# Kernel optimization log

Hardware: AMD Instinct MI355X
Metric: run time of the kernel (lower is better)

Reference implementation:

```python
import jax, jax.numpy as jnp
import numpy as np

NUM_CLASSES = 21
EPS = 1e-6
MOMENTUM = 0.99
K_WEAK = 16
K_STRONG = 256
PROB_THRESH = 0.95
IGNORE = 255
NEG = -1e30


def _normalize(x, axis=-1):
    # matches F.normalize(p=2) / CosineSimilarity with eps=1e-6
    n = jnp.linalg.norm(x, axis=axis, keepdims=True)
    return x / jnp.maximum(n, EPS)


def setup_inputs() -> dict:
    key = jax.random.key(0)
    k0, k1, k2, k3, k4, k5 = jax.random.split(key, 6)
    B, C, H, W = 8, 256, 128, 128
    feature_weak = jax.random.normal(k0, (B, C, H, W), jnp.float32)
    feature_strong = jax.random.normal(k1, (B, C, H, W), jnp.float32)
    probablity_weak = jax.random.uniform(k2, (B, H, W), jnp.float32)
    memory_bank = jax.random.normal(k3, (NUM_CLASSES, 1, C), jnp.float32)
    pred_weak = jax.random.randint(k4, (B, H, W), 0, NUM_CLASSES)
    ignore_mask = jax.random.randint(k5, (B, H, W), 0, 256)
    return {
        'feature_weak': feature_weak,
        'feature_strong': feature_strong,
        'probablity_weak': probablity_weak,
        'memory_bank': memory_bank,
        'pred_weak': pred_weak,
        'ignore_mask': ignore_mask,
    }


def reference(feature_weak, feature_strong, probablity_weak, memory_bank, pred_weak, ignore_mask):
    B, C, H, W = feature_weak.shape
    N = B * H * W
    fw = feature_weak.transpose(0, 2, 3, 1).reshape(N, C)   # weak pixel feats
    fs = feature_strong.transpose(0, 2, 3, 1).reshape(N, C) # strong pixel feats
    seg = pred_weak.reshape(N)
    ign = ignore_mask.reshape(N)  # same-size bilinear resize (align_corners) is identity
    prob = probablity_weak.reshape(N)

    valid = ign != IGNORE
    conf = valid & (prob > PROB_THRESH)

    cls = jnp.arange(NUM_CLASSES)
    is_cls = seg[None, :] == cls[:, None]        # [K, N]
    m_weak = is_cls & conf[None, :]              # per-class high-confidence mask
    m_strong = is_cls & valid[None, :]
    n_weak = m_weak.sum(axis=1)                  # [K]
    n_strong = m_strong.sum(axis=1)

    protos = memory_bank[:, 0, :]                # [K, C]
    pn = _normalize(protos)
    sim_w = _normalize(fw) @ pn.T                # [N, K] cos(pixel_weak, proto)
    sim_s = _normalize(fs) @ pn.T                # [N, K] cos(pixel_strong, proto)

    sw = jnp.where(m_weak, sim_w.T, NEG)         # [K, N]
    ss = jnp.where(m_strong, -sim_s.T, NEG)      # negate -> bottom-k via top_k
    _, idx_w = jax.lax.top_k(sw, K_WEAK)         # [K, 16] most-similar weak pixels
    _, idx_s = jax.lax.top_k(ss, K_STRONG)       # [K, 256] least-similar strong pixels

    # select_feature duplicates the top element: slots are ranks [0,0,1,...,14]
    ranks = jnp.maximum(jnp.arange(K_WEAK) - 1, 0)
    sel_w = fw[idx_w[:, ranks]]                  # [K, 16, C]
    sel_s = fs[idx_s]                            # [K, 256, C]

    kw = jnp.minimum(K_WEAK, n_weak)
    ks = jnp.minimum(K_STRONG, n_strong)
    valid_w = jnp.arange(K_WEAK)[None, :] < kw[:, None]     # [K, 16]
    valid_s = jnp.arange(K_STRONG)[None, :] < ks[:, None]   # [K, 256]

    # calculate_loss: weak side detached, max over strong dim, sum / strong count
    wn = _normalize(jax.lax.stop_gradient(sel_w))
    sn = _normalize(sel_s)
    cosm = jnp.einsum('kwc,ksc->kws', wn, sn)    # [K, 16, 256]
    cosm = jnp.where(valid_s[:, None, :], cosm, NEG)
    max_sim = jnp.where(valid_w, cosm.max(axis=2), 0.0)     # [K, 16]
    class_ok = (n_weak > 0) & (n_strong > 0)
    sim_sum = jnp.where(class_ok, max_sim.sum(axis=1), 0.0).sum()
    count = jnp.where(class_ok, ks, 0).sum()
    loss = jnp.where(count > 0, 1.0 - sim_sum / count, 0.0)

    # update_memory: per-class mean of high-confidence weak feats, EMA scatter
    fw_ng = jax.lax.stop_gradient(fw)            # .data copy -> no grad
    wsum = m_weak.astype(fw.dtype) @ fw_ng       # [K, C] segmented sum
    mean = wsum / jnp.maximum(n_weak, 1).astype(fw.dtype)[:, None]
    new_protos = jnp.where((n_weak > 0)[:, None],
                           MOMENTUM * protos + (1.0 - MOMENTUM) * mean,
                           protos)
    new_memory_bank = new_protos[:, None, :]     # [K, 1, C]
    return loss, new_memory_bank
```

## Files before the change

### kernel.cpp

```cpp
#include <hip/hip_runtime.h>
#include <stdint.h>

#define NCLS  21
#define CDIM  256
#define HWSZ  16384
#define NPIX  131072
#define EPSV  1e-6f
#define NEGV  -1e30f
#define CAP_W 4096
#define CAP_S 16384
#define KSEL  256
#define NCC   8
#define CCH   (CDIM/NCC)
#define NPART 8
#define NBLK2 (NPIX/512)
#define P2    2048
#define NPG   (NPIX/P2)

__device__ __forceinline__ uint64_t pack_key(float v, unsigned idx) {
  unsigned u = __float_as_uint(v);
  u = (u & 0x80000000u) ? ~u : (u | 0x80000000u);
  return ((uint64_t)(~u) << 32) | (uint64_t)idx;
}

__global__ void k0_init(const float* __restrict__ mb, float* pn, float* wsum) {
  int k = blockIdx.x, t = threadIdx.x;
  float v = mb[k * CDIM + t];
  float s = v * v;
  for (int o = 32; o > 0; o >>= 1) s += __shfl_down(s, o, 64);
  __shared__ float wsh[4];
  int wid = t >> 6, lane = t & 63;
  if (lane == 0) wsh[wid] = s;
  __syncthreads();
  float tot = wsh[0] + wsh[1] + wsh[2] + wsh[3];
  float inv = 1.0f / fmaxf(sqrtf(tot), EPSV);
  pn[k * CDIM + t] = v * inv;
  wsum[k * CDIM + t] = 0.0f;
}

__global__ __launch_bounds__(256, 2)
void k1a_stream(const float* __restrict__ fw, const float* __restrict__ fs,
                const float* __restrict__ prob, const int* __restrict__ seg,
                const int* __restrict__ ign, const float* __restrict__ pn,
                float* part, float* wsum) {
  __shared__ float pnT[CCH * NCLS];
  __shared__ float wloc[NCLS * (CCH + 1)];
  int t = threadIdx.x;
  int pg = blockIdx.x;
  int cc = blockIdx.y;
  int c0 = cc * CCH;
  for (int i = t; i < CCH * NCLS; i += 256) {
    int c = i / NCLS, k = i % NCLS;
    pnT[i] = pn[k * CDIM + c0 + c];
  }
  for (int i = t; i < NCLS * (CCH + 1); i += 256) wloc[i] = 0.0f;
  __syncthreads();

  int base = pg * P2;
  int b = base >> 14;
  int hwb = (base & (HWSZ - 1)) + t;

  int sgv[8]; bool cf[8];
  float dw[8], nw[8], dsv[8], nsv[8];
#pragma unroll
  for (int i = 0; i < 8; ++i) {
    int px = base + i * 256 + t;
    sgv[i] = seg[px];
    int igv = ign[px];
    float prv = prob[px];
    cf[i] = (igv != 255) && (prv > 0.95f);
    dw[i] = nw[i] = dsv[i] = nsv[i] = 0.0f;
  }

  const float* fwp = fw + ((size_t)b * CDIM + c0) * HWSZ + hwb;
  const float* fsp = fs + ((size_t)b * CDIM + c0) * HWSZ + hwb;

#pragma unroll 4
  for (int c = 0; c < CCH; ++c) {
    size_t co = (size_t)c * HWSZ;
    float a[8], s8[8];
#pragma unroll
    for (int i = 0; i < 8; ++i) a[i] = fwp[co + i * 256];
#pragma unroll
    for (int i = 0; i < 8; ++i) s8[i] = fsp[co + i * 256];
#pragma unroll
    for (int i = 0; i < 8; ++i) {
      float p = pnT[c * NCLS + sgv[i]];
      dw[i]  = fmaf(a[i],  p,     dw[i]);
      nw[i]  = fmaf(a[i],  a[i],  nw[i]);
      dsv[i] = fmaf(s8[i], p,     dsv[i]);
      nsv[i] = fmaf(s8[i], s8[i], nsv[i]);
      if (cf[i]) atomicAdd(&wloc[sgv[i] * (CCH + 1) + c], a[i]);
    }
  }

  float4* pp = (float4*)part + (size_t)cc * NPIX + base + t;
#pragma unroll
  for (int i = 0; i < 8; ++i)
    pp[i * 256] = make_float4(dw[i], nw[i], dsv[i], nsv[i]);

  __syncthreads();
  for (int i = t; i < NCLS * CCH; i += 256) {
    int k = i / CCH, cl = i % CCH;
    float v = wloc[k * (CCH + 1) + cl];
    if (v != 0.0f) atomicAdd(&wsum[k * CDIM + c0 + cl], v);
  }
}

__global__ void k1c_count(const float* __restrict__ prob, const int* __restrict__ seg,
                          const int* __restrict__ ign, int* cnts) {
  __shared__ int hs[NCLS], hw2[NCLS];
  int t = threadIdx.x, pg = blockIdx.x;
  for (int i = t; i < NCLS; i += 256) { hs[i] = 0; hw2[i] = 0; }
  __syncthreads();
  int n0 = pg * 512 + t * 2;
  int2   sg = *(const int2*)(seg + n0);
  int2   ig = *(const int2*)(ign + n0);
  float2 pr = *(const float2*)(prob + n0);
  bool v0 = (ig.x != 255), v1 = (ig.y != 255);
  if (v0) atomicAdd(&hs[sg.x], 1);
  if (v1) atomicAdd(&hs[sg.y], 1);
  if (v0 && pr.x > 0.95f) atomicAdd(&hw2[sg.x], 1);
  if (v1 && pr.y > 0.95f) atomicAdd(&hw2[sg.y], 1);
  __syncthreads();
  for (int i = t; i < NCLS; i += 256) {
    cnts[pg * NCLS + i] = hs[i];
    cnts[NBLK2 * NCLS + pg * NCLS + i] = hw2[i];
  }
}

__global__ void ks_scan(const int* __restrict__ cnts, int* offs, int* scnt, int* wcnt) {
  __shared__ int L[2 * NBLK2 * NCLS];
  int t = threadIdx.x;
  for (int i = t; i < 2 * NBLK2 * NCLS; i += 256) L[i] = cnts[i];
  __syncthreads();
  if (t < 2 * NCLS) {
    int q = t % NCLS;
    int typ = t / NCLS;
    int base = typ * NBLK2 * NCLS;
    int run = 0;
    for (int b2 = 0; b2 < NBLK2; ++b2) {
      int v = L[base + b2 * NCLS + q];
      L[base + b2 * NCLS + q] = run;
      run += v;
    }
    if (typ == 0) scnt[q] = run; else wcnt[q] = run;
  }
  __syncthreads();
  for (int i = t; i < 2 * NBLK2 * NCLS; i += 256) offs[i] = L[i];
}

__global__ void k1b_write(const float* __restrict__ part, const float* __restrict__ prob,
                          const int* __restrict__ seg, const int* __restrict__ ign,
                          const int* __restrict__ offs, uint64_t* wkeys, uint64_t* skeys) {
  __shared__ int ls[NCLS], lw[NCLS];
  int t = threadIdx.x, pg = blockIdx.x;
  if (t < NCLS) {
    ls[t] = offs[pg * NCLS + t];
    lw[t] = offs[NBLK2 * NCLS + pg * NCLS + t];
  }
  __syncthreads();
  int n0 = pg * 512 + t * 2;
  int2   sg = *(const int2*)(seg + n0);
  int2   ig = *(const int2*)(ign + n0);
  float2 pr = *(const float2*)(prob + n0);
  float dw[2] = {0,0}, nw[2] = {0,0}, ds[2] = {0,0}, ns[2] = {0,0};
#pragma unroll
  for (int cc = 0; cc < NCC; ++cc) {
    const float4* pp = (const float4*)part + ((size_t)cc * NPIX + n0);
#pragma unroll
    for (int i = 0; i < 2; ++i) {
      float4 v = pp[i];
      dw[i] += v.x; nw[i] += v.y; ds[i] += v.z; ns[i] += v.w;
    }
  }
  int   sga[2] = {sg.x, sg.y};
  int   iga[2] = {ig.x, ig.y};
  float pra[2] = {pr.x, pr.y};
#pragma unroll
  for (int i = 0; i < 2; ++i) {
    if (iga[i] != 255) {
      int q = sga[i];
      float sim_s = ds[i] / fmaxf(sqrtf(ns[i]), EPSV);
      int pos = atomicAdd(&ls[q], 1);
      if (pos < CAP_S) skeys[(size_t)q * CAP_S + pos] = pack_key(-sim_s, (unsigned)(n0 + i));
      if (pra[i] > 0.95f) {
        float sim_w = dw[i] / fmaxf(sqrtf(nw[i]), EPSV);
        int pw = atomicAdd(&lw[q], 1);
        if (pw < CAP_W) wkeys[(size_t)q * CAP_W + pw] = pack_key(sim_w, (unsigned)(n0 + i));
      }
    }
  }
}

__device__ void select_topk(const uint64_t* __restrict__ list, int cnt,
                            uint64_t* T, uint64_t* P, int* pcnt, int* woff) {
  int t = threadIdx.x;
  T[t] = ~0ull;
  if (t == 0) *pcnt = 0;
  __syncthreads();
  for (int base = 0; base < cnt; base += 256) {
    uint64_t key = (base + t < cnt) ? list[base + t] : ~0ull;
    uint64_t cutoff = T[KSEL - 1];
    bool pred = key < cutoff;
    unsigned long long mask = __ballot(pred);
    int wid = t >> 6, lane = t & 63;
    if (lane == 0) woff[wid] = __popcll(mask);
    int prefix = __popcll(mask & ((1ull << lane) - 1ull));
    __syncthreads();
    int off = 0;
    for (int w2 = 0; w2 < wid; ++w2) off += woff[w2];
    int total = woff[0] + woff[1] + woff[2] + woff[3];
    int old = *pcnt;
    if (pred) P[old + off + prefix] = key;
    int newc = old + total;
    __syncthreads();
    if (t == 0) *pcnt = newc;
    bool last = (base + 256 >= cnt);
    if (newc >= KSEL || (last && newc > 0)) {
      for (int i2 = t; i2 < 2 * KSEL; i2 += 256)
        if (i2 >= newc) P[i2] = ~0ull;
      for (unsigned size = 2; size <= 2 * KSEL; size <<= 1) {
        for (unsigned stride = size >> 1; stride > 0; stride >>= 1) {
          __syncthreads();
          unsigned lo = stride - 1;
          unsigned i = (((unsigned)t & ~lo) << 1) | ((unsigned)t & lo);
          unsigned j = i | stride;
          uint64_t a = P[i], b = P[j];
          bool up = ((i & size) == 0);
          if ((a > b) == up) { P[i] = b; P[j] = a; }
        }
      }
      __syncthreads();
      uint64_t a = T[t], b = P[KSEL - 1 - t];
      T[t] = a < b ? a : b;
      for (unsigned stride = KSEL / 2; stride > 0; stride >>= 1) {
        __syncthreads();
        if (((unsigned)t & stride) == 0) {
          uint64_t x = T[t], y = T[t + stride];
          if (x > y) { T[t] = y; T[t + stride] = x; }
        }
      }
      __syncthreads();
      if (t == 0) *pcnt = 0;
      __syncthreads();
    } else {
      __syncthreads();
    }
  }
}

__global__ void k2_topk(const uint64_t* __restrict__ wkeys, const uint64_t* __restrict__ skeys,
                        const int* wcnt, const int* scnt,
                        uint64_t* psel, int* idxw, int* kwv, int* nwv) {
  __shared__ uint64_t T[KSEL];
  __shared__ uint64_t P[2 * KSEL];
  __shared__ int pcnt;
  __shared__ int woff[4];
  int bid = blockIdx.x, t = threadIdx.x;
  if (bid < NCLS * NPART) {
    int k = bid / NPART, p = bid % NPART;
    int cnt = min(scnt[k], CAP_S);
    int chunk = (cnt + NPART - 1) / NPART;
    int lo = p * chunk;
    int hi = min(lo + chunk, cnt);
    int c = hi > lo ? hi - lo : 0;
    select_topk(skeys + (size_t)k * CAP_S + lo, c, T, P, &pcnt, woff);
    psel[((size_t)k * NPART + p) * KSEL + t] = T[t];
  } else {
    int k = bid - NCLS * NPART;
    int cnt_total = wcnt[k];
    int cnt = min(cnt_total, CAP_W);
    select_topk(wkeys + (size_t)k * CAP_W, cnt, T, P, &pcnt, woff);
    if (t < 16) idxw[k * 16 + t] = (int)(unsigned)(T[t] & 0xFFFFFFFFull);
    if (t == 0) { nwv[k] = cnt_total; kwv[k] = min(cnt_total, 16); }
  }
}

__global__ void k2m_merge(const uint64_t* __restrict__ psel, const int* scnt,
                          int* idxs, int* ksv, int* nsv) {
  int k = blockIdx.x, t = threadIdx.x;
  __shared__ uint64_t M[NPART * KSEL];
  __shared__ uint64_t M2[4 * KSEL];
  for (int i = t; i < NPART * KSEL; i += 256) M[i] = psel[(size_t)k * NPART * KSEL + i];
  __syncthreads();
#pragma unroll
  for (int p = 0; p < 4; ++p) {
    uint64_t a = M[p * 512 + t], b = M[p * 512 + 511 - t];
    M2[p * 256 + t] = a < b ? a : b;
  }
  for (int str = 128; str > 0; str >>= 1) {
    __syncthreads();
    for (int q = t; q < 4 * 128; q += 256) {
      int list = q >> 7, r = q & 127;
      int i = ((r & ~(str - 1)) << 1) | (r & (str - 1));
      int ai = list * 256 + i, bi = ai + str;
      uint64_t x = M2[ai], y = M2[bi];
      if (x > y) { M2[ai] = y; M2[bi] = x; }
    }
  }
  __syncthreads();
#pragma unroll
  for (int p = 0; p < 2; ++p) {
    uint64_t a = M2[p * 512 + t], b = M2[p * 512 + 511 - t];
    M[p * 256 + t] = a < b ? a : b;
  }
  for (int str = 128; str > 0; str >>= 1) {
    __syncthreads();
    {
      int q = t;
      int list = q >> 7, r = q & 127;
      int i = ((r & ~(str - 1)) << 1) | (r & (str - 1));
      int ai = list * 256 + i, bi = ai + str;
      uint64_t x = M[ai], y = M[bi];
      if (x > y) { M[ai] = y; M[bi] = x; }
    }
  }
  __syncthreads();
  {
    uint64_t a = M[t], b = M[511 - t];
    M2[t] = a < b ? a : b;
  }
  for (int str = 128; str > 0; str >>= 1) {
    __syncthreads();
    if (t < 128) {
      int r = t;
      int i = ((r & ~(str - 1)) << 1) | (r & (str - 1));
      uint64_t x = M2[i], y = M2[i + str];
      if (x > y) { M2[i] = y; M2[i + str] = x; }
    }
  }
  __syncthreads();
  idxs[k * KSEL + t] = (int)(unsigned)(M2[t] & 0xFFFFFFFFull);
  if (t == 0) { int c = scnt[k]; nsv[k] = c; ksv[k] = c < KSEL ? c : KSEL; }
}

__global__ void k3a_gather(const float* __restrict__ fw, const float* __restrict__ fs,
                           const int* __restrict__ idxw, const int* __restrict__ idxs,
                           const int* __restrict__ kwv, const int* __restrict__ ksv,
                           float* dw_dense, float* ds_dense) {
  int k = blockIdx.y;
  int s0 = blockIdx.x * 4;
  int t = threadIdx.x;
  int wid = t >> 6, lane = t & 63;
  float v[4];
  bool strong[4];
  int slot_[4];
#pragma unroll
  for (int j = 0; j < 4; ++j) {
    int slot = s0 + j;
    slot_[j] = slot;
    strong[j] = slot < KSEL;
    bool ok;
    int n = 0;
    if (strong[j]) {
      ok = slot < ksv[k];
      if (ok) n = idxs[k * KSEL + slot];
    } else {
      int i = slot - KSEL;
      ok = i < kwv[k];
      int rank = i > 0 ? i - 1 : 0;
      if (ok) n = idxw[k * 16 + rank];
    }
    v[j] = 0.0f;
    if (ok) {
      int b = n >> 14, hw = n & (HWSZ - 1);
      const float* f = strong[j] ? fs : fw;
      v[j] = f[(size_t)(b * CDIM + t) * HWSZ + hw];
    }
  }
  __shared__ float wsh[4][4];
  float s[4];
#pragma unroll
  for (int j = 0; j < 4; ++j) {
    s[j] = v[j] * v[j];
    for (int o = 32; o > 0; o >>= 1) s[j] += __shfl_down(s[j], o, 64);
  }
  if (lane == 0) {
#pragma unroll
    for (int j = 0; j < 4; ++j) wsh[wid][j] = s[j];
  }
  __syncthreads();
#pragma unroll
  for (int j = 0; j < 4; ++j) {
    float tot = wsh[0][j] + wsh[1][j] + wsh[2][j] + wsh[3][j];
    float inv = 1.0f / fmaxf(sqrtf(tot), EPSV);
    float out = v[j] * inv;
    if (strong[j]) ds_dense[((size_t)k * KSEL + slot_[j]) * CDIM + t] = out;
    else           dw_dense[((size_t)k * 16 + (slot_[j] - KSEL)) * CDIM + t] = out;
  }
}

__global__ void k3b_loss(const float* __restrict__ dw_dense, const float* __restrict__ ds_dense,
                         const int* kwv, const int* ksv, const int* nwv, const int* nsv,
                         float* simsum, int* countk) {
  int k = blockIdx.x, t = threadIdx.x;
  int wid = t >> 6, lane = t & 63;
  __shared__ float wn[16 * CDIM];
  __shared__ float wred[4][16];
  for (int i = t; i < 16 * CDIM; i += 256) wn[i] = dw_dense[(size_t)k * 16 * CDIM + i];
  __syncthreads();
  int ks_ = ksv[k], kw_ = kwv[k];
  bool ok = (nwv[k] > 0) && (nsv[k] > 0);
  float dots[16];
#pragma unroll
  for (int i = 0; i < 16; ++i) dots[i] = 0.0f;
  bool jv = ok && (t < ks_);
  if (jv) {
    const float4* sp = (const float4*)(ds_dense + ((size_t)k * KSEL + t) * CDIM);
    for (int c4 = 0; c4 < CDIM / 4; ++c4) {
      float4 v = sp[c4];
#pragma unroll
      for (int i = 0; i < 16; ++i) {
        float4 w = ((const float4*)(wn + i * CDIM))[c4];
        dots[i] = fmaf(v.x, w.x, dots[i]);
        dots[i] = fmaf(v.y, w.y, dots[i]);
        dots[i] = fmaf(v.z, w.z, dots[i]);
        dots[i] = fmaf(v.w, w.w, dots[i]);
      }
    }
  }
#pragma unroll
  for (int i = 0; i < 16; ++i) {
    float v = jv ? dots[i] : NEGV;
    for (int o = 32; o > 0; o >>= 1) v = fmaxf(v, __shfl_down(v, o, 64));
    if (lane == 0) wred[wid][i] = v;
  }
  __syncthreads();
  if (t == 0) {
    float csum = 0.0f;
    for (int i = 0; i < kw_; ++i) {
      float m = fmaxf(fmaxf(wred[0][i], wred[1][i]), fmaxf(wred[2][i], wred[3][i]));
      csum += m;
    }
    simsum[k] = ok ? csum : 0.0f;
    countk[k] = ok ? ks_ : 0;
  }
}

__global__ void k4_final(const float* __restrict__ mb, const float* __restrict__ wsum,
                         const int* __restrict__ nwv, const float* __restrict__ simsum,
                         const int* __restrict__ countk, float* out) {
  int k = blockIdx.x, t = threadIdx.x;
  float p = mb[k * CDIM + t];
  float o = p;
  int nw = nwv[k];
  if (nw > 0) {
    float mean = wsum[k * CDIM + t] / (float)nw;
    o = 0.99f * p + 0.01f * mean;
  }
  out[1 + k * CDIM + t] = o;
  if (k == 0 && t == 0) {
    float ss = 0.0f;
    int cc = 0;
    for (int q = 0; q < NCLS; ++q) { ss += simsum[q]; cc += countk[q]; }
    out[0] = (cc > 0) ? (1.0f - ss / (float)cc) : 0.0f;
  }
}

extern "C" void kernel_launch(void* const* d_in, const int* in_sizes, int n_in,
                              void* d_out, int out_size, void* d_ws, size_t ws_size,
                              hipStream_t stream) {
  const float* fw   = (const float*)d_in[0];
  const float* fs   = (const float*)d_in[1];
  const float* prob = (const float*)d_in[2];
  const float* mb   = (const float*)d_in[3];
  const int*   seg  = (const int*)d_in[4];
  const int*   ign  = (const int*)d_in[5];
  float* out = (float*)d_out;

  char* ws = (char*)d_ws;
  size_t off = 0;
  auto alloc = [&](size_t bytes) -> char* {
    char* p = ws + off;
    off = (off + bytes + 255) & ~(size_t)255;
    return p;
  };
  float*    pn       = (float*)alloc(NCLS * CDIM * 4);
  float*    wsum     = (float*)alloc(NCLS * CDIM * 4);
  int*      wcnt     = (int*)alloc(NCLS * 4);
  int*      scnt     = (int*)alloc(NCLS * 4);
  int*      idxw     = (int*)alloc(NCLS * 16 * 4);
  int*      idxs     = (int*)alloc(NCLS * KSEL * 4);
  int*      kwv      = (int*)alloc(NCLS * 4);
  int*      ksv      = (int*)alloc(NCLS * 4);
  int*      nwv      = (int*)alloc(NCLS * 4);
  int*      nsv      = (int*)alloc(NCLS * 4);
  float*    simsum   = (float*)alloc(NCLS * 4);
  int*      countk   = (int*)alloc(NCLS * 4);
  int*      cnts     = (int*)alloc(2 * NBLK2 * NCLS * 4);
  int*      offs     = (int*)alloc(2 * NBLK2 * NCLS * 4);
  uint64_t* wkeys    = (uint64_t*)alloc((size_t)NCLS * CAP_W * 8);
  uint64_t* skeys    = (uint64_t*)alloc((size_t)NCLS * CAP_S * 8);
  uint64_t* psel     = (uint64_t*)alloc((size_t)NCLS * NPART * KSEL * 8);
  float*    dw_dense = (float*)alloc((size_t)NCLS * 16 * CDIM * 4);
  float*    ds_dense = (float*)alloc((size_t)NCLS * KSEL * CDIM * 4);
  float*    part     = (float*)alloc((size_t)NCC * NPIX * 4 * 4);
  (void)in_sizes; (void)n_in; (void)out_size; (void)ws_size;

  k0_init<<<NCLS, 256, 0, stream>>>(mb, pn, wsum);
  k1a_stream<<<dim3(NPG, NCC), 256, 0, stream>>>(fw, fs, prob, seg, ign, pn,
                                                 part, wsum);
  k1c_count<<<NBLK2, 256, 0, stream>>>(prob, seg, ign, cnts);
  ks_scan<<<1, 256, 0, stream>>>(cnts, offs, scnt, wcnt);
  k1b_write<<<NBLK2, 256, 0, stream>>>(part, prob, seg, ign, offs, wkeys, skeys);
  k2_topk<<<NCLS * NPART + NCLS, 256, 0, stream>>>(wkeys, skeys, wcnt, scnt,
                                                   psel, idxw, kwv, nwv);
  k2m_merge<<<NCLS, 256, 0, stream>>>(psel, scnt, idxs, ksv, nsv);
  k3a_gather<<<dim3((KSEL + 16) / 4, NCLS), 256, 0, stream>>>(fw, fs, idxw, idxs, kwv, ksv,
                                                              dw_dense, ds_dense);
  k3b_loss<<<NCLS, 256, 0, stream>>>(dw_dense, ds_dense, kwv, ksv, nwv, nsv,
                                     simsum, countk);
  k4_final<<<NCLS, 256, 0, stream>>>(mb, wsum, nwv, simsum, countk, out);
}
```

Measured before the change: 403.1 us.

## Fuse streaming, counting, scan and key-write into one kernel with atomic offsets

The channel-chunked streaming kernel, the per-block histogram, the single-block scan and the key-writing pass are merged into one kernel. Each block now processes 512 pixels across all 256 channels and claims per-class output slots through global atomics instead of a precomputed prefix scan. This removes the partial-dot-product buffer round trip and several launches. The loss step is also split across 4 smaller blocks per class, with the final reduction moved into the last kernel. In exchange the grid shrinks to 256 blocks with a long serial channel loop and roughly 43KB of shared memory per block, which may limit occupancy and memory-latency hiding. Key order within each class list becomes nondeterministic, though top-k ties break on pixel index.

```diff
diff --git a/kernel.cpp b/kernel.cpp
--- a/kernel.cpp
+++ b/kernel.cpp
@@ -10,12 +10,10 @@
 #define CAP_W 4096
 #define CAP_S 16384
 #define KSEL  256
-#define NCC   8
-#define CCH   (CDIM/NCC)
 #define NPART 8
-#define NBLK2 (NPIX/512)
-#define P2    2048
-#define NPG   (NPIX/P2)
+#define P2M   512
+#define NBLKM (NPIX/P2M)
+#define CPAD  (CDIM+1)
 
 __device__ __forceinline__ uint64_t pack_key(float v, unsigned idx) {
   unsigned u = __float_as_uint(v);
@@ -23,7 +21,8 @@
   return ((uint64_t)(~u) << 32) | (uint64_t)idx;
 }
 
-__global__ void k0_init(const float* __restrict__ mb, float* pn, float* wsum) {
+__global__ void k0_init(const float* __restrict__ mb, float* pn, float* wsum,
+                        int* wcnt, int* scnt) {
   int k = blockIdx.x, t = threadIdx.x;
   float v = mb[k * CDIM + t];
   float s = v * v;
@@ -36,160 +35,96 @@
   float inv = 1.0f / fmaxf(sqrtf(tot), EPSV);
   pn[k * CDIM + t] = v * inv;
   wsum[k * CDIM + t] = 0.0f;
-}
-
-__global__ __launch_bounds__(256, 2)
-void k1a_stream(const float* __restrict__ fw, const float* __restrict__ fs,
-                const float* __restrict__ prob, const int* __restrict__ seg,
-                const int* __restrict__ ign, const float* __restrict__ pn,
-                float* part, float* wsum) {
-  __shared__ float pnT[CCH * NCLS];
-  __shared__ float wloc[NCLS * (CCH + 1)];
-  int t = threadIdx.x;
-  int pg = blockIdx.x;
-  int cc = blockIdx.y;
-  int c0 = cc * CCH;
-  for (int i = t; i < CCH * NCLS; i += 256) {
+  if (k == 0 && t < 2 * NCLS) {
+    if (t < NCLS) wcnt[t] = 0; else scnt[t - NCLS] = 0;
+  }
+}
+
+__global__ __launch_bounds__(256)
+void k1a_mega(const float* __restrict__ fw, const float* __restrict__ fs,
+              const float* __restrict__ prob, const int* __restrict__ seg,
+              const int* __restrict__ ign, const float* __restrict__ pn,
+              float* wsum, int* wcnt, int* scnt,
+              uint64_t* wkeys, uint64_t* skeys) {
+  __shared__ float pnT[CDIM * NCLS];
+  __shared__ float wloc[NCLS * CPAD];
+  __shared__ int cw[NCLS], cs[NCLS], bw[NCLS], bs[NCLS];
+  int t = threadIdx.x, pg = blockIdx.x;
+  for (int i = t; i < CDIM * NCLS; i += 256) {
     int c = i / NCLS, k = i % NCLS;
-    pnT[i] = pn[k * CDIM + c0 + c];
-  }
-  for (int i = t; i < NCLS * (CCH + 1); i += 256) wloc[i] = 0.0f;
-  __syncthreads();
-
-  int base = pg * P2;
+    pnT[i] = pn[k * CDIM + c];
+  }
+  for (int i = t; i < NCLS * CPAD; i += 256) wloc[i] = 0.0f;
+  if (t < NCLS) { cw[t] = 0; cs[t] = 0; }
+  __syncthreads();
+
+  int base = pg * P2M;
   int b = base >> 14;
-  int hwb = (base & (HWSZ - 1)) + t;
-
-  int sgv[8]; bool cf[8];
-  float dw[8], nw[8], dsv[8], nsv[8];
-#pragma unroll
-  for (int i = 0; i < 8; ++i) {
-    int px = base + i * 256 + t;
-    sgv[i] = seg[px];
-    int igv = ign[px];
-    float prv = prob[px];
-    cf[i] = (igv != 255) && (prv > 0.95f);
-    dw[i] = nw[i] = dsv[i] = nsv[i] = 0.0f;
-  }
-
-  const float* fwp = fw + ((size_t)b * CDIM + c0) * HWSZ + hwb;
-  const float* fsp = fs + ((size_t)b * CDIM + c0) * HWSZ + hwb;
-
-#pragma unroll 4
-  for (int c = 0; c < CCH; ++c) {
-    size_t co = (size_t)c * HWSZ;
-    float a[8], s8[8];
-#pragma unroll
-    for (int i = 0; i < 8; ++i) a[i] = fwp[co + i * 256];
-#pragma unroll
-    for (int i = 0; i < 8; ++i) s8[i] = fsp[co + i * 256];
-#pragma unroll
-    for (int i = 0; i < 8; ++i) {
-      float p = pnT[c * NCLS + sgv[i]];
-      dw[i]  = fmaf(a[i],  p,     dw[i]);
-      nw[i]  = fmaf(a[i],  a[i],  nw[i]);
-      dsv[i] = fmaf(s8[i], p,     dsv[i]);
-      nsv[i] = fmaf(s8[i], s8[i], nsv[i]);
-      if (cf[i]) atomicAdd(&wloc[sgv[i] * (CCH + 1) + c], a[i]);
-    }
-  }
-
-  float4* pp = (float4*)part + (size_t)cc * NPIX + base + t;
-#pragma unroll
-  for (int i = 0; i < 8; ++i)
-    pp[i * 256] = make_float4(dw[i], nw[i], dsv[i], nsv[i]);
-
-  __syncthreads();
-  for (int i = t; i < NCLS * CCH; i += 256) {
-    int k = i / CCH, cl = i % CCH;
-    float v = wloc[k * (CCH + 1) + cl];
-    if (v != 0.0f) atomicAdd(&wsum[k * CDIM + c0 + cl], v);
-  }
-}
-
-__global__ void k1c_count(const float* __restrict__ prob, const int* __restrict__ seg,
-                          const int* __restrict__ ign, int* cnts) {
-  __shared__ int hs[NCLS], hw2[NCLS];
-  int t = threadIdx.x, pg = blockIdx.x;
-  for (int i = t; i < NCLS; i += 256) { hs[i] = 0; hw2[i] = 0; }
-  __syncthreads();
-  int n0 = pg * 512 + t * 2;
-  int2   sg = *(const int2*)(seg + n0);
-  int2   ig = *(const int2*)(ign + n0);
-  float2 pr = *(const float2*)(prob + n0);
-  bool v0 = (ig.x != 255), v1 = (ig.y != 255);
-  if (v0) atomicAdd(&hs[sg.x], 1);
-  if (v1) atomicAdd(&hs[sg.y], 1);
-  if (v0 && pr.x > 0.95f) atomicAdd(&hw2[sg.x], 1);
-  if (v1 && pr.y > 0.95f) atomicAdd(&hw2[sg.y], 1);
-  __syncthreads();
-  for (int i = t; i < NCLS; i += 256) {
-    cnts[pg * NCLS + i] = hs[i];
-    cnts[NBLK2 * NCLS + pg * NCLS + i] = hw2[i];
-  }
-}
-
-__global__ void ks_scan(const int* __restrict__ cnts, int* offs, int* scnt, int* wcnt) {
-  __shared__ int L[2 * NBLK2 * NCLS];
-  int t = threadIdx.x;
-  for (int i = t; i < 2 * NBLK2 * NCLS; i += 256) L[i] = cnts[i];
-  __syncthreads();
-  if (t < 2 * NCLS) {
-    int q = t % NCLS;
-    int typ = t / NCLS;
-    int base = typ * NBLK2 * NCLS;
-    int run = 0;
-    for (int b2 = 0; b2 < NBLK2; ++b2) {
-      int v = L[base + b2 * NCLS + q];
-      L[base + b2 * NCLS + q] = run;
-      run += v;
-    }
-    if (typ == 0) scnt[q] = run; else wcnt[q] = run;
-  }
-  __syncthreads();
-  for (int i = t; i < 2 * NBLK2 * NCLS; i += 256) offs[i] = L[i];
-}
-
-__global__ void k1b_write(const float* __restrict__ part, const float* __restrict__ prob,
-                          const int* __restrict__ seg, const int* __restrict__ ign,
-                          const int* __restrict__ offs, uint64_t* wkeys, uint64_t* skeys) {
-  __shared__ int ls[NCLS], lw[NCLS];
-  int t = threadIdx.x, pg = blockIdx.x;
+  int hw0 = (base & (HWSZ - 1)) + t;
+  int n0 = base + t, n1 = base + 256 + t;
+  int sg0 = seg[n0], sg1 = seg[n1];
+  int ig0 = ign[n0], ig1 = ign[n1];
+  float pr0 = prob[n0], pr1 = prob[n1];
+  bool va0 = (ig0 != 255), va1 = (ig1 != 255);
+  bool cf0 = va0 && (pr0 > 0.95f), cf1 = va1 && (pr1 > 0.95f);
+
+  const float* fwp = fw + (size_t)b * CDIM * HWSZ + hw0;
+  const float* fsp = fs + (size_t)b * CDIM * HWSZ + hw0;
+
+  float dw0 = 0, nw0 = 0, ds0 = 0, ns0 = 0;
+  float dw1 = 0, nw1 = 0, ds1 = 0, ns1 = 0;
+#pragma unroll 8
+  for (int c = 0; c < CDIM; ++c) {
+    size_t o = (size_t)c * HWSZ;
+    float a0 = __builtin_nontemporal_load(fwp + o);
+    float a1 = __builtin_nontemporal_load(fwp + o + 256);
+    float s0 = __builtin_nontemporal_load(fsp + o);
+    float s1 = __builtin_nontemporal_load(fsp + o + 256);
+    float p0 = pnT[c * NCLS + sg0];
+    float p1 = pnT[c * NCLS + sg1];
+    dw0 = fmaf(a0, p0, dw0); nw0 = fmaf(a0, a0, nw0);
+    ds0 = fmaf(s0, p0, ds0); ns0 = fmaf(s0, s0, ns0);
+    dw1 = fmaf(a1, p1, dw1); nw1 = fmaf(a1, a1, nw1);
+    ds1 = fmaf(s1, p1, ds1); ns1 = fmaf(s1, s1, ns1);
+    if (cf0) atomicAdd(&wloc[sg0 * CPAD + c], a0);
+    if (cf1) atomicAdd(&wloc[sg1 * CPAD + c], a1);
+  }
+
+  int ls0 = 0, lw0 = 0, ls1 = 0, lw1 = 0;
+  if (va0) ls0 = atomicAdd(&cs[sg0], 1);
+  if (va1) ls1 = atomicAdd(&cs[sg1], 1);
+  if (cf0) lw0 = atomicAdd(&cw[sg0], 1);
+  if (cf1) lw1 = atomicAdd(&cw[sg1], 1);
+  __syncthreads();
   if (t < NCLS) {
-    ls[t] = offs[pg * NCLS + t];
-    lw[t] = offs[NBLK2 * NCLS + pg * NCLS + t];
-  }
-  __syncthreads();
-  int n0 = pg * 512 + t * 2;
-  int2   sg = *(const int2*)(seg + n0);
-  int2   ig = *(const int2*)(ign + n0);
-  float2 pr = *(const float2*)(prob + n0);
-  float dw[2] = {0,0}, nw[2] = {0,0}, ds[2] = {0,0}, ns[2] = {0,0};
-#pragma unroll
-  for (int cc = 0; cc < NCC; ++cc) {
-    const float4* pp = (const float4*)part + ((size_t)cc * NPIX + n0);
-#pragma unroll
-    for (int i = 0; i < 2; ++i) {
-      float4 v = pp[i];
-      dw[i] += v.x; nw[i] += v.y; ds[i] += v.z; ns[i] += v.w;
-    }
-  }
-  int   sga[2] = {sg.x, sg.y};
-  int   iga[2] = {ig.x, ig.y};
-  float pra[2] = {pr.x, pr.y};
-#pragma unroll
-  for (int i = 0; i < 2; ++i) {
-    if (iga[i] != 255) {
-      int q = sga[i];
-      float sim_s = ds[i] / fmaxf(sqrtf(ns[i]), EPSV);
-      int pos = atomicAdd(&ls[q], 1);
-      if (pos < CAP_S) skeys[(size_t)q * CAP_S + pos] = pack_key(-sim_s, (unsigned)(n0 + i));
-      if (pra[i] > 0.95f) {
-        float sim_w = dw[i] / fmaxf(sqrtf(nw[i]), EPSV);
-        int pw = atomicAdd(&lw[q], 1);
-        if (pw < CAP_W) wkeys[(size_t)q * CAP_W + pw] = pack_key(sim_w, (unsigned)(n0 + i));
-      }
-    }
+    bs[t] = atomicAdd(&scnt[t], cs[t]);
+    bw[t] = atomicAdd(&wcnt[t], cw[t]);
+  }
+  __syncthreads();
+  if (va0) {
+    float sim_s = ds0 / fmaxf(sqrtf(ns0), EPSV);
+    int pos = bs[sg0] + ls0;
+    if (pos < CAP_S) skeys[(size_t)sg0 * CAP_S + pos] = pack_key(-sim_s, (unsigned)n0);
+    if (cf0) {
+      float sim_w = dw0 / fmaxf(sqrtf(nw0), EPSV);
+      int pw = bw[sg0] + lw0;
+      if (pw < CAP_W) wkeys[(size_t)sg0 * CAP_W + pw] = pack_key(sim_w, (unsigned)n0);
+    }
+  }
+  if (va1) {
+    float sim_s = ds1 / fmaxf(sqrtf(ns1), EPSV);
+    int pos = bs[sg1] + ls1;
+    if (pos < CAP_S) skeys[(size_t)sg1 * CAP_S + pos] = pack_key(-sim_s, (unsigned)n1);
+    if (cf1) {
+      float sim_w = dw1 / fmaxf(sqrtf(nw1), EPSV);
+      int pw = bw[sg1] + lw1;
+      if (pw < CAP_W) wkeys[(size_t)sg1 * CAP_W + pw] = pack_key(sim_w, (unsigned)n1);
+    }
+  }
+  for (int i = t; i < NCLS * CDIM; i += 256) {
+    int k = i >> 8, c = i & 255;
+    float v = wloc[k * CPAD + c];
+    if (v != 0.0f) atomicAdd(&wsum[k * CDIM + c], v);
   }
 }
 
@@ -252,7 +187,7 @@
 
 __global__ void k2_topk(const uint64_t* __restrict__ wkeys, const uint64_t* __restrict__ skeys,
                         const int* wcnt, const int* scnt,
-                        uint64_t* psel, int* idxw, int* kwv, int* nwv) {
+                        uint64_t* psel, int* idxw) {
   __shared__ uint64_t T[KSEL];
   __shared__ uint64_t P[2 * KSEL];
   __shared__ int pcnt;
@@ -269,16 +204,13 @@
     psel[((size_t)k * NPART + p) * KSEL + t] = T[t];
   } else {
     int k = bid - NCLS * NPART;
-    int cnt_total = wcnt[k];
-    int cnt = min(cnt_total, CAP_W);
+    int cnt = min(wcnt[k], CAP_W);
     select_topk(wkeys + (size_t)k * CAP_W, cnt, T, P, &pcnt, woff);
     if (t < 16) idxw[k * 16 + t] = (int)(unsigned)(T[t] & 0xFFFFFFFFull);
-    if (t == 0) { nwv[k] = cnt_total; kwv[k] = min(cnt_total, 16); }
-  }
-}
-
-__global__ void k2m_merge(const uint64_t* __restrict__ psel, const int* scnt,
-                          int* idxs, int* ksv, int* nsv) {
+  }
+}
+
+__global__ void k2m_merge(const uint64_t* __restrict__ psel, int* idxs) {
   int k = blockIdx.x, t = threadIdx.x;
   __shared__ uint64_t M[NPART * KSEL];
   __shared__ uint64_t M2[4 * KSEL];
@@ -332,17 +264,18 @@
   }
   __syncthreads();
   idxs[k * KSEL + t] = (int)(unsigned)(M2[t] & 0xFFFFFFFFull);
-  if (t == 0) { int c = scnt[k]; nsv[k] = c; ksv[k] = c < KSEL ? c : KSEL; }
 }
 
 __global__ void k3a_gather(const float* __restrict__ fw, const float* __restrict__ fs,
                            const int* __restrict__ idxw, const int* __restrict__ idxs,
-                           const int* __restrict__ kwv, const int* __restrict__ ksv,
+                           const int* __restrict__ wcnt, const int* __restrict__ scnt,
                            float* dw_dense, float* ds_dense) {
   int k = blockIdx.y;
   int s0 = blockIdx.x * 4;
   int t = threadIdx.x;
   int wid = t >> 6, lane = t & 63;
+  int kw_ = min(wcnt[k], 16);
+  int ks_ = min(scnt[k], KSEL);
   float v[4];
   bool strong[4];
   int slot_[4];
@@ -354,11 +287,11 @@
     bool ok;
     int n = 0;
     if (strong[j]) {
-      ok = slot < ksv[k];
+      ok = slot < ks_;
       if (ok) n = idxs[k * KSEL + slot];
     } else {
       int i = slot - KSEL;
-      ok = i < kwv[k];
+      ok = i < kw_;
       int rank = i > 0 ? i - 1 : 0;
       if (ok) n = idxw[k * 16 + rank];
     }
@@ -392,22 +325,19 @@
 }
 
 __global__ void k3b_loss(const float* __restrict__ dw_dense, const float* __restrict__ ds_dense,
-                         const int* kwv, const int* ksv, const int* nwv, const int* nsv,
-                         float* simsum, int* countk) {
-  int k = blockIdx.x, t = threadIdx.x;
-  int wid = t >> 6, lane = t & 63;
+                         const int* __restrict__ scnt, float* pmax) {
+  int p = blockIdx.x, k = blockIdx.y, t = threadIdx.x;
   __shared__ float wn[16 * CDIM];
-  __shared__ float wred[4][16];
-  for (int i = t; i < 16 * CDIM; i += 256) wn[i] = dw_dense[(size_t)k * 16 * CDIM + i];
-  __syncthreads();
-  int ks_ = ksv[k], kw_ = kwv[k];
-  bool ok = (nwv[k] > 0) && (nsv[k] > 0);
+  for (int i = t; i < 16 * CDIM; i += 64) wn[i] = dw_dense[(size_t)k * 16 * CDIM + i];
+  __syncthreads();
+  int ks_ = min(scnt[k], KSEL);
+  int slot = p * 64 + t;
+  bool jv = slot < ks_;
   float dots[16];
 #pragma unroll
   for (int i = 0; i < 16; ++i) dots[i] = 0.0f;
-  bool jv = ok && (t < ks_);
   if (jv) {
-    const float4* sp = (const float4*)(ds_dense + ((size_t)k * KSEL + t) * CDIM);
+    const float4* sp = (const float4*)(ds_dense + ((size_t)k * KSEL + slot) * CDIM);
     for (int c4 = 0; c4 < CDIM / 4; ++c4) {
       float4 v = sp[c4];
 #pragma unroll
@@ -424,37 +354,50 @@
   for (int i = 0; i < 16; ++i) {
     float v = jv ? dots[i] : NEGV;
     for (int o = 32; o > 0; o >>= 1) v = fmaxf(v, __shfl_down(v, o, 64));
-    if (lane == 0) wred[wid][i] = v;
-  }
-  __syncthreads();
-  if (t == 0) {
-    float csum = 0.0f;
-    for (int i = 0; i < kw_; ++i) {
-      float m = fmaxf(fmaxf(wred[0][i], wred[1][i]), fmaxf(wred[2][i], wred[3][i]));
-      csum += m;
-    }
-    simsum[k] = ok ? csum : 0.0f;
-    countk[k] = ok ? ks_ : 0;
+    if (t == 0) pmax[((size_t)k * 4 + p) * 16 + i] = v;
   }
 }
 
 __global__ void k4_final(const float* __restrict__ mb, const float* __restrict__ wsum,
-                         const int* __restrict__ nwv, const float* __restrict__ simsum,
-                         const int* __restrict__ countk, float* out) {
+                         const int* __restrict__ wcnt, const int* __restrict__ scnt,
+                         const float* __restrict__ pmax, float* out) {
   int k = blockIdx.x, t = threadIdx.x;
   float p = mb[k * CDIM + t];
   float o = p;
-  int nw = nwv[k];
+  int nw = wcnt[k];
   if (nw > 0) {
     float mean = wsum[k * CDIM + t] / (float)nw;
     o = 0.99f * p + 0.01f * mean;
   }
   out[1 + k * CDIM + t] = o;
-  if (k == 0 && t == 0) {
-    float ss = 0.0f;
-    int cc = 0;
-    for (int q = 0; q < NCLS; ++q) { ss += simsum[q]; cc += countk[q]; }
-    out[0] = (cc > 0) ? (1.0f - ss / (float)cc) : 0.0f;
+  if (k == 0) {
+    __shared__ float stot;
+    __shared__ int ctot;
+    if (t == 0) { stot = 0.0f; ctot = 0; }
+    __syncthreads();
+    float part = 0.0f;
+    int cpart = 0;
+    for (int idx = t; idx < NCLS * 16; idx += 256) {
+      int q = idx >> 4, i = idx & 15;
+      int nwq = wcnt[q], nsq = scnt[q];
+      if (nwq > 0 && nsq > 0 && i < min(nwq, 16)) {
+        float m =    pmax[((size_t)q * 4 + 0) * 16 + i];
+        m = fmaxf(m, pmax[((size_t)q * 4 + 1) * 16 + i]);
+        m = fmaxf(m, pmax[((size_t)q * 4 + 2) * 16 + i]);
+        m = fmaxf(m, pmax[((size_t)q * 4 + 3) * 16 + i]);
+        part += m;
+      }
+    }
+    if (t < NCLS) {
+      if (wcnt[t] > 0 && scnt[t] > 0) cpart = min(scnt[t], KSEL);
+    }
+    for (int o2 = 32; o2 > 0; o2 >>= 1) {
+      part += __shfl_down(part, o2, 64);
+      cpart += __shfl_down(cpart, o2, 64);
+    }
+    if ((t & 63) == 0) { atomicAdd(&stot, part); atomicAdd(&ctot, cpart); }
+    __syncthreads();
+    if (t == 0) out[0] = (ctot > 0) ? (1.0f - stot / (float)ctot) : 0.0f;
   }
 }
 
@@ -482,34 +425,23 @@
   int*      scnt     = (int*)alloc(NCLS * 4);
   int*      idxw     = (int*)alloc(NCLS * 16 * 4);
   int*      idxs     = (int*)alloc(NCLS * KSEL * 4);
-  int*      kwv      = (int*)alloc(NCLS * 4);
-  int*      ksv      = (int*)alloc(NCLS * 4);
-  int*      nwv      = (int*)alloc(NCLS * 4);
-  int*      nsv      = (int*)alloc(NCLS * 4);
-  float*    simsum   = (float*)alloc(NCLS * 4);
-  int*      countk   = (int*)alloc(NCLS * 4);
-  int*      cnts     = (int*)alloc(2 * NBLK2 * NCLS * 4);
-  int*      offs     = (int*)alloc(2 * NBLK2 * NCLS * 4);
+  float*    pmax     = (float*)alloc(NCLS * 4 * 16 * 4);
   uint64_t* wkeys    = (uint64_t*)alloc((size_t)NCLS * CAP_W * 8);
   uint64_t* skeys    = (uint64_t*)alloc((size_t)NCLS * CAP_S * 8);
   uint64_t* psel     = (uint64_t*)alloc((size_t)NCLS * NPART * KSEL * 8);
   float*    dw_dense = (float*)alloc((size_t)NCLS * 16 * CDIM * 4);
   float*    ds_dense = (float*)alloc((size_t)NCLS * KSEL * CDIM * 4);
-  float*    part     = (float*)alloc((size_t)NCC * NPIX * 4 * 4);
   (void)in_sizes; (void)n_in; (void)out_size; (void)ws_size;
 
-  k0_init<<<NCLS, 256, 0, stream>>>(mb, pn, wsum);
-  k1a_stream<<<dim3(NPG, NCC), 256, 0, stream>>>(fw, fs, prob, seg, ign, pn,
-                                                 part, wsum);
-  k1c_count<<<NBLK2, 256, 0, stream>>>(prob, seg, ign, cnts);
-  ks_scan<<<1, 256, 0, stream>>>(cnts, offs, scnt, wcnt);
-  k1b_write<<<NBLK2, 256, 0, stream>>>(part, prob, seg, ign, offs, wkeys, skeys);
+  k0_init<<<NCLS, 256, 0, stream>>>(mb, pn, wsum, wcnt, scnt);
+  k1a_mega<<<NBLKM, 256, 0, stream>>>(fw, fs, prob, seg, ign, pn,
+                                      wsum, wcnt, scnt, wkeys, skeys);
   k2_topk<<<NCLS * NPART + NCLS, 256, 0, stream>>>(wkeys, skeys, wcnt, scnt,
-                                                   psel, idxw, kwv, nwv);
-  k2m_merge<<<NCLS, 256, 0, stream>>>(psel, scnt, idxs, ksv, nsv);
-  k3a_gather<<<dim3((KSEL + 16) / 4, NCLS), 256, 0, stream>>>(fw, fs, idxw, idxs, kwv, ksv,
+                                                   psel, idxw);
+  k2m_merge<<<NCLS, 256, 0, stream>>>(psel, idxs);
+  k3a_gather<<<dim3((KSEL + 16) / 4, NCLS), 256, 0, stream>>>(fw, fs, idxw, idxs,
+                                                              wcnt, scnt,
                                                               dw_dense, ds_dense);
-  k3b_loss<<<NCLS, 256, 0, stream>>>(dw_dense, ds_dense, kwv, ksv, nwv, nsv,
-                                     simsum, countk);
-  k4_final<<<NCLS, 256, 0, stream>>>(mb, wsum, nwv, simsum, countk, out);
-}
+  k3b_loss<<<dim3(4, NCLS), 64, 0, stream>>>(dw_dense, ds_dense, scnt, pmax);
+  k4_final<<<NCLS, 256, 0, stream>>>(mb, wsum, wcnt, scnt, pmax, out);
+}
```

Measured after the change: 444.1 us. +10.2%, slower.

## Replace count/scan kernels with atomic block offsets and split loss reduction

Applied to the files above, without the earlier changes.

Drops the separate per-block histogram and prefix-scan kernels. k1b_write now counts locally in shared memory and reserves its per-class output ranges with global atomics on counters that k0_init zeroes. The loss kernel is split into 4 blocks of 64 threads per class, and the final max and sum over those partials moves into k4_final, which also removes the small metadata arrays. Key ordering within each class list becomes nondeterministic, but top-k selection keys still carry the pixel index, so the selected set should not change.

```diff
diff --git a/kernel.cpp b/kernel.cpp
--- a/kernel.cpp
+++ b/kernel.cpp
@@ -23,7 +23,8 @@
   return ((uint64_t)(~u) << 32) | (uint64_t)idx;
 }
 
-__global__ void k0_init(const float* __restrict__ mb, float* pn, float* wsum) {
+__global__ void k0_init(const float* __restrict__ mb, float* pn, float* wsum,
+                        int* wcnt, int* scnt) {
   int k = blockIdx.x, t = threadIdx.x;
   float v = mb[k * CDIM + t];
   float s = v * v;
@@ -36,6 +37,9 @@
   float inv = 1.0f / fmaxf(sqrtf(tot), EPSV);
   pn[k * CDIM + t] = v * inv;
   wsum[k * CDIM + t] = 0.0f;
+  if (k == 0 && t < 2 * NCLS) {
+    if (t < NCLS) wcnt[t] = 0; else scnt[t - NCLS] = 0;
+  }
 }
 
 __global__ __launch_bounds__(256, 2)
@@ -107,58 +111,12 @@
   }
 }
 
-__global__ void k1c_count(const float* __restrict__ prob, const int* __restrict__ seg,
-                          const int* __restrict__ ign, int* cnts) {
-  __shared__ int hs[NCLS], hw2[NCLS];
-  int t = threadIdx.x, pg = blockIdx.x;
-  for (int i = t; i < NCLS; i += 256) { hs[i] = 0; hw2[i] = 0; }
-  __syncthreads();
-  int n0 = pg * 512 + t * 2;
-  int2   sg = *(const int2*)(seg + n0);
-  int2   ig = *(const int2*)(ign + n0);
-  float2 pr = *(const float2*)(prob + n0);
-  bool v0 = (ig.x != 255), v1 = (ig.y != 255);
-  if (v0) atomicAdd(&hs[sg.x], 1);
-  if (v1) atomicAdd(&hs[sg.y], 1);
-  if (v0 && pr.x > 0.95f) atomicAdd(&hw2[sg.x], 1);
-  if (v1 && pr.y > 0.95f) atomicAdd(&hw2[sg.y], 1);
-  __syncthreads();
-  for (int i = t; i < NCLS; i += 256) {
-    cnts[pg * NCLS + i] = hs[i];
-    cnts[NBLK2 * NCLS + pg * NCLS + i] = hw2[i];
-  }
-}
-
-__global__ void ks_scan(const int* __restrict__ cnts, int* offs, int* scnt, int* wcnt) {
-  __shared__ int L[2 * NBLK2 * NCLS];
-  int t = threadIdx.x;
-  for (int i = t; i < 2 * NBLK2 * NCLS; i += 256) L[i] = cnts[i];
-  __syncthreads();
-  if (t < 2 * NCLS) {
-    int q = t % NCLS;
-    int typ = t / NCLS;
-    int base = typ * NBLK2 * NCLS;
-    int run = 0;
-    for (int b2 = 0; b2 < NBLK2; ++b2) {
-      int v = L[base + b2 * NCLS + q];
-      L[base + b2 * NCLS + q] = run;
-      run += v;
-    }
-    if (typ == 0) scnt[q] = run; else wcnt[q] = run;
-  }
-  __syncthreads();
-  for (int i = t; i < 2 * NBLK2 * NCLS; i += 256) offs[i] = L[i];
-}
-
 __global__ void k1b_write(const float* __restrict__ part, const float* __restrict__ prob,
                           const int* __restrict__ seg, const int* __restrict__ ign,
-                          const int* __restrict__ offs, uint64_t* wkeys, uint64_t* skeys) {
-  __shared__ int ls[NCLS], lw[NCLS];
+                          int* wcnt, int* scnt, uint64_t* wkeys, uint64_t* skeys) {
+  __shared__ int cs[NCLS], cw[NCLS], bs[NCLS], bw[NCLS];
   int t = threadIdx.x, pg = blockIdx.x;
-  if (t < NCLS) {
-    ls[t] = offs[pg * NCLS + t];
-    lw[t] = offs[NBLK2 * NCLS + pg * NCLS + t];
-  }
+  for (int i = t; i < NCLS; i += 256) { cs[i] = 0; cw[i] = 0; }
   __syncthreads();
   int n0 = pg * 512 + t * 2;
   int2   sg = *(const int2*)(seg + n0);
@@ -177,16 +135,31 @@
   int   sga[2] = {sg.x, sg.y};
   int   iga[2] = {ig.x, ig.y};
   float pra[2] = {pr.x, pr.y};
+  bool  va[2], cfv[2];
+  int   lsl[2] = {0,0}, lwl[2] = {0,0};
 #pragma unroll
   for (int i = 0; i < 2; ++i) {
-    if (iga[i] != 255) {
+    va[i]  = (iga[i] != 255);
+    cfv[i] = va[i] && (pra[i] > 0.95f);
+    if (va[i])  lsl[i] = atomicAdd(&cs[sga[i]], 1);
+    if (cfv[i]) lwl[i] = atomicAdd(&cw[sga[i]], 1);
+  }
+  __syncthreads();
+  if (t < NCLS) {
+    bs[t] = atomicAdd(&scnt[t], cs[t]);
+    bw[t] = atomicAdd(&wcnt[t], cw[t]);
+  }
+  __syncthreads();
+#pragma unroll
+  for (int i = 0; i < 2; ++i) {
+    if (va[i]) {
       int q = sga[i];
       float sim_s = ds[i] / fmaxf(sqrtf(ns[i]), EPSV);
-      int pos = atomicAdd(&ls[q], 1);
+      int pos = bs[q] + lsl[i];
       if (pos < CAP_S) skeys[(size_t)q * CAP_S + pos] = pack_key(-sim_s, (unsigned)(n0 + i));
-      if (pra[i] > 0.95f) {
+      if (cfv[i]) {
         float sim_w = dw[i] / fmaxf(sqrtf(nw[i]), EPSV);
-        int pw = atomicAdd(&lw[q], 1);
+        int pw = bw[q] + lwl[i];
         if (pw < CAP_W) wkeys[(size_t)q * CAP_W + pw] = pack_key(sim_w, (unsigned)(n0 + i));
       }
     }
@@ -252,7 +225,7 @@
 
 __global__ void k2_topk(const uint64_t* __restrict__ wkeys, const uint64_t* __restrict__ skeys,
                         const int* wcnt, const int* scnt,
-                        uint64_t* psel, int* idxw, int* kwv, int* nwv) {
+                        uint64_t* psel, int* idxw) {
   __shared__ uint64_t T[KSEL];
   __shared__ uint64_t P[2 * KSEL];
   __shared__ int pcnt;
@@ -269,16 +242,13 @@
     psel[((size_t)k * NPART + p) * KSEL + t] = T[t];
   } else {
     int k = bid - NCLS * NPART;
-    int cnt_total = wcnt[k];
-    int cnt = min(cnt_total, CAP_W);
+    int cnt = min(wcnt[k], CAP_W);
     select_topk(wkeys + (size_t)k * CAP_W, cnt, T, P, &pcnt, woff);
     if (t < 16) idxw[k * 16 + t] = (int)(unsigned)(T[t] & 0xFFFFFFFFull);
-    if (t == 0) { nwv[k] = cnt_total; kwv[k] = min(cnt_total, 16); }
-  }
-}
-
-__global__ void k2m_merge(const uint64_t* __restrict__ psel, const int* scnt,
-                          int* idxs, int* ksv, int* nsv) {
+  }
+}
+
+__global__ void k2m_merge(const uint64_t* __restrict__ psel, int* idxs) {
   int k = blockIdx.x, t = threadIdx.x;
   __shared__ uint64_t M[NPART * KSEL];
   __shared__ uint64_t M2[4 * KSEL];
@@ -332,17 +302,18 @@
   }
   __syncthreads();
   idxs[k * KSEL + t] = (int)(unsigned)(M2[t] & 0xFFFFFFFFull);
-  if (t == 0) { int c = scnt[k]; nsv[k] = c; ksv[k] = c < KSEL ? c : KSEL; }
 }
 
 __global__ void k3a_gather(const float* __restrict__ fw, const float* __restrict__ fs,
                            const int* __restrict__ idxw, const int* __restrict__ idxs,
-                           const int* __restrict__ kwv, const int* __restrict__ ksv,
+                           const int* __restrict__ wcnt, const int* __restrict__ scnt,
                            float* dw_dense, float* ds_dense) {
   int k = blockIdx.y;
   int s0 = blockIdx.x * 4;
   int t = threadIdx.x;
   int wid = t >> 6, lane = t & 63;
+  int kw_ = min(wcnt[k], 16);
+  int ks_ = min(scnt[k], KSEL);
   float v[4];
   bool strong[4];
   int slot_[4];
@@ -354,11 +325,11 @@
     bool ok;
     int n = 0;
     if (strong[j]) {
-      ok = slot < ksv[k];
+      ok = slot < ks_;
       if (ok) n = idxs[k * KSEL + slot];
     } else {
       int i = slot - KSEL;
-      ok = i < kwv[k];
+      ok = i < kw_;
       int rank = i > 0 ? i - 1 : 0;
       if (ok) n = idxw[k * 16 + rank];
     }
@@ -392,22 +363,19 @@
 }
 
 __global__ void k3b_loss(const float* __restrict__ dw_dense, const float* __restrict__ ds_dense,
-                         const int* kwv, const int* ksv, const int* nwv, const int* nsv,
-                         float* simsum, int* countk) {
-  int k = blockIdx.x, t = threadIdx.x;
-  int wid = t >> 6, lane = t & 63;
+                         const int* __restrict__ scnt, float* pmax) {
+  int p = blockIdx.x, k = blockIdx.y, t = threadIdx.x;
   __shared__ float wn[16 * CDIM];
-  __shared__ float wred[4][16];
-  for (int i = t; i < 16 * CDIM; i += 256) wn[i] = dw_dense[(size_t)k * 16 * CDIM + i];
-  __syncthreads();
-  int ks_ = ksv[k], kw_ = kwv[k];
-  bool ok = (nwv[k] > 0) && (nsv[k] > 0);
+  for (int i = t; i < 16 * CDIM; i += 64) wn[i] = dw_dense[(size_t)k * 16 * CDIM + i];
+  __syncthreads();
+  int ks_ = min(scnt[k], KSEL);
+  int slot = p * 64 + t;
+  bool jv = slot < ks_;
   float dots[16];
 #pragma unroll
   for (int i = 0; i < 16; ++i) dots[i] = 0.0f;
-  bool jv = ok && (t < ks_);
   if (jv) {
-    const float4* sp = (const float4*)(ds_dense + ((size_t)k * KSEL + t) * CDIM);
+    const float4* sp = (const float4*)(ds_dense + ((size_t)k * KSEL + slot) * CDIM);
     for (int c4 = 0; c4 < CDIM / 4; ++c4) {
       float4 v = sp[c4];
 #pragma unroll
@@ -424,37 +392,50 @@
   for (int i = 0; i < 16; ++i) {
     float v = jv ? dots[i] : NEGV;
     for (int o = 32; o > 0; o >>= 1) v = fmaxf(v, __shfl_down(v, o, 64));
-    if (lane == 0) wred[wid][i] = v;
-  }
-  __syncthreads();
-  if (t == 0) {
-    float csum = 0.0f;
-    for (int i = 0; i < kw_; ++i) {
-      float m = fmaxf(fmaxf(wred[0][i], wred[1][i]), fmaxf(wred[2][i], wred[3][i]));
-      csum += m;
-    }
-    simsum[k] = ok ? csum : 0.0f;
-    countk[k] = ok ? ks_ : 0;
+    if (t == 0) pmax[((size_t)k * 4 + p) * 16 + i] = v;
   }
 }
 
 __global__ void k4_final(const float* __restrict__ mb, const float* __restrict__ wsum,
-                         const int* __restrict__ nwv, const float* __restrict__ simsum,
-                         const int* __restrict__ countk, float* out) {
+                         const int* __restrict__ wcnt, const int* __restrict__ scnt,
+                         const float* __restrict__ pmax, float* out) {
   int k = blockIdx.x, t = threadIdx.x;
   float p = mb[k * CDIM + t];
   float o = p;
-  int nw = nwv[k];
+  int nw = wcnt[k];
   if (nw > 0) {
     float mean = wsum[k * CDIM + t] / (float)nw;
     o = 0.99f * p + 0.01f * mean;
   }
   out[1 + k * CDIM + t] = o;
-  if (k == 0 && t == 0) {
-    float ss = 0.0f;
-    int cc = 0;
-    for (int q = 0; q < NCLS; ++q) { ss += simsum[q]; cc += countk[q]; }
-    out[0] = (cc > 0) ? (1.0f - ss / (float)cc) : 0.0f;
+  if (k == 0) {
+    __shared__ float stot;
+    __shared__ int ctot;
+    if (t == 0) { stot = 0.0f; ctot = 0; }
+    __syncthreads();
+    float part = 0.0f;
+    int cpart = 0;
+    for (int idx = t; idx < NCLS * 16; idx += 256) {
+      int q = idx >> 4, i = idx & 15;
+      int nwq = wcnt[q], nsq = scnt[q];
+      if (nwq > 0 && nsq > 0 && i < min(nwq, 16)) {
+        float m =    pmax[((size_t)q * 4 + 0) * 16 + i];
+        m = fmaxf(m, pmax[((size_t)q * 4 + 1) * 16 + i]);
+        m = fmaxf(m, pmax[((size_t)q * 4 + 2) * 16 + i]);
+        m = fmaxf(m, pmax[((size_t)q * 4 + 3) * 16 + i]);
+        part += m;
+      }
+    }
+    if (t < NCLS) {
+      if (wcnt[t] > 0 && scnt[t] > 0) cpart = min(scnt[t], KSEL);
+    }
+    for (int o2 = 32; o2 > 0; o2 >>= 1) {
+      part += __shfl_down(part, o2, 64);
+      cpart += __shfl_down(cpart, o2, 64);
+    }
+    if ((t & 63) == 0) { atomicAdd(&stot, part); atomicAdd(&ctot, cpart); }
+    __syncthreads();
+    if (t == 0) out[0] = (ctot > 0) ? (1.0f - stot / (float)ctot) : 0.0f;
   }
 }
 
@@ -482,14 +463,7 @@
   int*      scnt     = (int*)alloc(NCLS * 4);
   int*      idxw     = (int*)alloc(NCLS * 16 * 4);
   int*      idxs     = (int*)alloc(NCLS * KSEL * 4);
-  int*      kwv      = (int*)alloc(NCLS * 4);
-  int*      ksv      = (int*)alloc(NCLS * 4);
-  int*      nwv      = (int*)alloc(NCLS * 4);
-  int*      nsv      = (int*)alloc(NCLS * 4);
-  float*    simsum   = (float*)alloc(NCLS * 4);
-  int*      countk   = (int*)alloc(NCLS * 4);
-  int*      cnts     = (int*)alloc(2 * NBLK2 * NCLS * 4);
-  int*      offs     = (int*)alloc(2 * NBLK2 * NCLS * 4);
+  float*    pmax     = (float*)alloc(NCLS * 4 * 16 * 4);
   uint64_t* wkeys    = (uint64_t*)alloc((size_t)NCLS * CAP_W * 8);
   uint64_t* skeys    = (uint64_t*)alloc((size_t)NCLS * CAP_S * 8);
   uint64_t* psel     = (uint64_t*)alloc((size_t)NCLS * NPART * KSEL * 8);
@@ -498,18 +472,17 @@
   float*    part     = (float*)alloc((size_t)NCC * NPIX * 4 * 4);
   (void)in_sizes; (void)n_in; (void)out_size; (void)ws_size;
 
-  k0_init<<<NCLS, 256, 0, stream>>>(mb, pn, wsum);
+  k0_init<<<NCLS, 256, 0, stream>>>(mb, pn, wsum, wcnt, scnt);
   k1a_stream<<<dim3(NPG, NCC), 256, 0, stream>>>(fw, fs, prob, seg, ign, pn,
                                                  part, wsum);
-  k1c_count<<<NBLK2, 256, 0, stream>>>(prob, seg, ign, cnts);
-  ks_scan<<<1, 256, 0, stream>>>(cnts, offs, scnt, wcnt);
-  k1b_write<<<NBLK2, 256, 0, stream>>>(part, prob, seg, ign, offs, wkeys, skeys);
+  k1b_write<<<NBLK2, 256, 0, stream>>>(part, prob, seg, ign, wcnt, scnt,
+                                       wkeys, skeys);
   k2_topk<<<NCLS * NPART + NCLS, 256, 0, stream>>>(wkeys, skeys, wcnt, scnt,
-                                                   psel, idxw, kwv, nwv);
-  k2m_merge<<<NCLS, 256, 0, stream>>>(psel, scnt, idxs, ksv, nsv);
-  k3a_gather<<<dim3((KSEL + 16) / 4, NCLS), 256, 0, stream>>>(fw, fs, idxw, idxs, kwv, ksv,
+                                                   psel, idxw);
+  k2m_merge<<<NCLS, 256, 0, stream>>>(psel, idxs);
+  k3a_gather<<<dim3((KSEL + 16) / 4, NCLS), 256, 0, stream>>>(fw, fs, idxw, idxs,
+                                                              wcnt, scnt,
                                                               dw_dense, ds_dense);
-  k3b_loss<<<NCLS, 256, 0, stream>>>(dw_dense, ds_dense, kwv, ksv, nwv, nsv,
-                                     simsum, countk);
-  k4_final<<<NCLS, 256, 0, stream>>>(mb, wsum, nwv, simsum, countk, out);
-}
+  k3b_loss<<<dim3(4, NCLS), 64, 0, stream>>>(dw_dense, ds_dense, scnt, pmax);
+  k4_final<<<NCLS, 256, 0, stream>>>(mb, wsum, wcnt, scnt, pmax, out);
+}
```

Result: faster. 392.5 us (-2.6%).
